# Kernel tuning notes

Hardware: AMD Instinct MI355X
Metric: run time of the kernel (lower is better)

The kernel has to match this reference:

```python
import jax, jax.numpy as jnp
import numpy as np

B, H, W, K, A = 4096, 32, 32, 20, 4


def setup_inputs() -> dict:
    key = jax.random.key(0)
    k_wall, k_agent, k_goal, k_phi, k_l1, k_l2 = jax.random.split(key, 6)
    # obs channels: 0 = wall/feature map (random), 1 = one-hot agent pos, 2 = one-hot goal pos
    walls = jax.random.uniform(k_wall, (B, H, W), dtype=jnp.float32)
    agent_idx = jax.random.randint(k_agent, (B,), 0, H * W)
    goal_idx = jax.random.randint(k_goal, (B,), 0, H * W)
    agent = jax.nn.one_hot(agent_idx, H * W, dtype=jnp.float32).reshape(B, H, W)
    goal = jax.nn.one_hot(goal_idx, H * W, dtype=jnp.float32).reshape(B, H, W)
    obs = jnp.stack([walls, agent, goal], axis=-1)  # (B,H,W,3)
    obs_flat = obs.reshape(B, H * W * 3)
    din = H * W * 3
    return {
        "obs_flat": obs_flat,
        "Phi_w": jax.random.normal(k_phi, (din, 2 * H * W), dtype=jnp.float32) * 0.02,
        "Phi_b": jnp.zeros((2 * H * W,), jnp.float32),
        "L1_w": jax.random.normal(k_l1, (36, 16), dtype=jnp.float32) * 0.1,
        "L1_b": jnp.zeros((16,), jnp.float32),
        "L2_w": jax.random.normal(k_l2, (16, A), dtype=jnp.float32) * 0.1,
        "L2_b": jnp.zeros((A,), jnp.float32),
    }


def _mvprop(r, p):
    # K-step value propagation: V <- max(V, r + p*(best 4-neighbor V - r))
    # p = sigmoid(...) >= 0, so max over the 4 shifted nv values equals nv of the max shift.
    def body(V, _):
        pv = jnp.pad(V, ((0, 0), (1, 1), (1, 1)))
        nbr = jnp.maximum(
            jnp.maximum(pv[:, :-2, 1:-1], pv[:, 2:, 1:-1]),   # up, down
            jnp.maximum(pv[:, 1:-1, :-2], pv[:, 1:-1, 2:]),   # left, right
        )
        return jnp.maximum(V, r + p * (nbr - r)), None
    V, _ = jax.lax.scan(body, r, None, length=K)
    return V


def reference(obs_flat, Phi_w, Phi_b, L1_w, L1_b, L2_w, L2_b):
    b = obs_flat.shape[0]
    obs = obs_flat.reshape(b, H, W, 3)
    phi = jax.nn.sigmoid(obs_flat @ Phi_w + Phi_b).reshape(b, H, W, 2)
    r, p = phi[..., 0], phi[..., 1]
    V = _mvprop(r, p)  # (b,H,W)
    obs_val = jnp.concatenate([obs, V[..., None]], axis=-1)  # (b,H,W,4)
    padded = jnp.pad(obs_val, ((0, 0), (1, 1), (1, 1), (0, 0)))
    # agent position: exactly one nonzero in channel 1 per sample -> argmax
    idx = jnp.argmax(obs[..., 1].reshape(b, -1), axis=1)
    pi, pj = idx // W, idx % W
    # 3x3 neighborhood around agent in padded grid (start = pos+1-1 = pos)
    def slice_one(ov, i, j):
        return jax.lax.dynamic_slice(ov, (i, j, 0), (3, 3, 4))
    sel = jax.vmap(slice_one)(padded, pi, pj)  # (b,3,3,4)
    h = jax.nn.relu(sel.reshape(b, 36) @ L1_w + L1_b)
    logit = h @ L2_w + L2_b
    return logit
```

## Files before the change

kernel.cpp:

```cpp
#include <hip/hip_runtime.h>
#include <hip/hip_fp16.h>

#define BATCH 4096
#define HH 32
#define WW 32
#define KPROP 20
#define NACT 4
#define DIN 3072
#define DPHI 2048
#define HWC 1024
#define KC 1024
#define TILE_ELEMS (16 * KC)

typedef _Float16 h8_t __attribute__((ext_vector_type(8)));
typedef _Float16 h4_t __attribute__((ext_vector_type(4)));
typedef float f32x4 __attribute__((ext_vector_type(4)));

__device__ inline float sigmoidf(float x) { return 1.0f / (1.0f + __expf(-x)); }

__device__ inline float dpp_shr1(float x) {
    return __int_as_float(__builtin_amdgcn_update_dpp(
        0, __float_as_int(x), 0x111, 0xF, 0xF, true));
}
__device__ inline float dpp_shl1(float x) {
    return __int_as_float(__builtin_amdgcn_update_dpp(
        0, __float_as_int(x), 0x101, 0xF, 0xF, true));
}

__device__ inline size_t pack_off(int row, int k) {
    return (size_t)(row >> 4) * TILE_ELEMS + (k >> 3) * 128 + (row & 15) * 8 + (k & 7);
}

__global__ __launch_bounds__(256) void prep_fused_kernel(
    const float* __restrict__ obs,
    const float* __restrict__ Phi_w,
    _Float16* __restrict__ A_pack,
    _Float16* __restrict__ B_pack,
    _Float16* __restrict__ Pag,
    int* __restrict__ aidx, int* __restrict__ gidx)
{
    if (blockIdx.x < BATCH) {
        const int t = blockIdx.x * 256 + threadIdx.x;
        const int b = t >> 8;
        const int c0 = (t & 255) * 4;
        const float* src = obs + (size_t)b * DIN + 3 * c0;
        const float4 f0 = *(const float4*)(src);
        const float4 f1 = *(const float4*)(src + 4);
        const float4 f2 = *(const float4*)(src + 8);
        h4_t w;
        w[0] = (_Float16)f0.x; w[1] = (_Float16)f0.w;
        w[2] = (_Float16)f1.z; w[3] = (_Float16)f2.y;
        *(h4_t*)(A_pack + pack_off(b, c0)) = w;
        if (f0.y > 0.5f) aidx[b] = c0;
        if (f1.x > 0.5f) aidx[b] = c0 + 1;
        if (f1.w > 0.5f) aidx[b] = c0 + 2;
        if (f2.z > 0.5f) aidx[b] = c0 + 3;
        if (f0.z > 0.5f) gidx[b] = c0;
        if (f1.y > 0.5f) gidx[b] = c0 + 1;
        if (f2.x > 0.5f) gidx[b] = c0 + 2;
        if (f2.w > 0.5f) gidx[b] = c0 + 3;
    } else {
        const int bid = blockIdx.x - BATCH;
        const int ni = bid & 63;
        const int ci = bid >> 6;
        const int tx = threadIdx.x & 31;
        const int ty = threadIdx.x >> 5;
        #pragma unroll
        for (int s = 0; s < 4; s++) {
            const int r = ty + 8 * s;
            const int c = ci * 32 + r;
            const int n = ni * 32 + tx;
            const float w0 = Phi_w[(size_t)(3 * c) * DPHI + n];
            Pag[(size_t)c * DPHI + n]         = (_Float16)Phi_w[(size_t)(3 * c + 1) * DPHI + n];
            Pag[(size_t)(HWC + c) * DPHI + n] = (_Float16)Phi_w[(size_t)(3 * c + 2) * DPHI + n];
            B_pack[pack_off(n, c)] = (_Float16)w0;
        }
    }
}

__global__ __launch_bounds__(256) void gemm_pre_kernel(
    const _Float16* __restrict__ A_pack,
    const _Float16* __restrict__ B_pack,
    const float* __restrict__ bias,
    _Float16* __restrict__ pre)
{
    const int tid  = threadIdx.x;
    const int lane = tid & 63;
    const int wid  = tid >> 6;
    const int m0 = blockIdx.y * 64;
    const int n0 = blockIdx.x * 256 + wid * 64;
    const int lm = lane & 15;
    const int kq = lane >> 4;

    const _Float16* Abase = A_pack + (size_t)(blockIdx.y * 4) * TILE_ELEMS + 8 * lane;
    const _Float16* Bbase = B_pack + (size_t)(blockIdx.x * 16 + wid * 4) * TILE_ELEMS + 8 * lane;

    f32x4 acc[4][4] = {};
    h8_t a0[4], b0[4], a1[4], b1[4];

    #pragma unroll
    for (int i = 0; i < 4; i++) {
        a0[i] = *(const h8_t*)(Abase + i * TILE_ELEMS);
        b0[i] = *(const h8_t*)(Bbase + i * TILE_ELEMS);
        a1[i] = *(const h8_t*)(Abase + i * TILE_ELEMS + 32 * 16);
        b1[i] = *(const h8_t*)(Bbase + i * TILE_ELEMS + 32 * 16);
    }

    for (int k0 = 0; k0 < KC; k0 += 64) {
        #pragma unroll
        for (int mt = 0; mt < 4; mt++)
            #pragma unroll
            for (int nt = 0; nt < 4; nt++)
                acc[mt][nt] = __builtin_amdgcn_mfma_f32_16x16x32_f16(
                    a0[mt], b0[nt], acc[mt][nt], 0, 0, 0);
        if (k0 + 64 < KC) {
            #pragma unroll
            for (int i = 0; i < 4; i++) {
                a0[i] = *(const h8_t*)(Abase + i * TILE_ELEMS + (k0 + 64) * 16);
                b0[i] = *(const h8_t*)(Bbase + i * TILE_ELEMS + (k0 + 64) * 16);
            }
        }
        #pragma unroll
        for (int mt = 0; mt < 4; mt++)
            #pragma unroll
            for (int nt = 0; nt < 4; nt++)
                acc[mt][nt] = __builtin_amdgcn_mfma_f32_16x16x32_f16(
                    a1[mt], b1[nt], acc[mt][nt], 0, 0, 0);
        if (k0 + 96 < KC) {
            #pragma unroll
            for (int i = 0; i < 4; i++) {
                a1[i] = *(const h8_t*)(Abase + i * TILE_ELEMS + (k0 + 96) * 16);
                b1[i] = *(const h8_t*)(Bbase + i * TILE_ELEMS + (k0 + 96) * 16);
            }
        }
    }

    #pragma unroll
    for (int nt = 0; nt < 4; nt++) {
        const int col = n0 + nt * 16 + lm;
        const float bcol = bias[col];
        #pragma unroll
        for (int mt = 0; mt < 4; mt++) {
            #pragma unroll
            for (int r = 0; r < 4; r++) {
                const int row = m0 + mt * 16 + kq * 4 + r;
                pre[(size_t)row * DPHI + col] = (_Float16)(acc[mt][nt][r] + bcol);
            }
        }
    }
}

__global__ __launch_bounds__(256, 4) void vprop_head_kernel(
    const _Float16* __restrict__ pre,
    const _Float16* __restrict__ Pag,
    const float* __restrict__ obs,
    const int* __restrict__ aidx,
    const int* __restrict__ gidx,
    const float* __restrict__ L1w,
    const float* __restrict__ L1b,
    const float* __restrict__ L2w,
    const float* __restrict__ L2b,
    float* __restrict__ out)
{
    __shared__ __align__(16) float Vg[4][HWC];
    __shared__ float sel[4][36], hbuf[4][16];

    const int tid  = threadIdx.x;
    const int w    = tid >> 6;
    const int lane = tid & 63;
    const int b    = blockIdx.x * 4 + w;
    const int bi   = lane & 15;
    const int bj   = lane >> 4;
    const int ai = aidx[b];
    const int gi = gidx[b];

    const _Float16* pb = pre + (size_t)b * DPHI;
    const _Float16* ra = Pag + (size_t)ai * DPHI;
    const _Float16* rg = Pag + (size_t)(HWC + gi) * DPHI;

    float v[2][8], p[2][8], a[2][8];
    #pragma unroll
    for (int r = 0; r < 2; r++) {
        const int off = 64 * (2 * bi + r) + 16 * bj;
        const h8_t ph0 = *(const h8_t*)(pb + off), ph1 = *(const h8_t*)(pb + off + 8);
        const h8_t pa0 = *(const h8_t*)(ra + off), pa1 = *(const h8_t*)(ra + off + 8);
        const h8_t pg0 = *(const h8_t*)(rg + off), pg1 = *(const h8_t*)(rg + off + 8);
        #pragma unroll
        for (int c = 0; c < 4; c++) {
            const float rv = sigmoidf((float)ph0[2*c]   + (float)pa0[2*c]   + (float)pg0[2*c]);
            const float pv = sigmoidf((float)ph0[2*c+1] + (float)pa0[2*c+1] + (float)pg0[2*c+1]);
            v[r][c] = rv; p[r][c] = pv; a[r][c] = rv * (1.0f - pv);
            const float rv2 = sigmoidf((float)ph1[2*c]   + (float)pa1[2*c]   + (float)pg1[2*c]);
            const float pv2 = sigmoidf((float)ph1[2*c+1] + (float)pa1[2*c+1] + (float)pg1[2*c+1]);
            v[r][c+4] = rv2; p[r][c+4] = pv2; a[r][c+4] = rv2 * (1.0f - pv2);
        }
    }

    for (int it = 0; it < KPROP; it++) {
        float uh[8], dh[8], lh[2], rh[2];
        #pragma unroll
        for (int c = 0; c < 8; c++) {
            uh[c] = dpp_shr1(v[1][c]);
            dh[c] = dpp_shl1(v[0][c]);
        }
        #pragma unroll
        for (int r = 0; r < 2; r++) {
            lh[r] = __shfl(v[r][7], lane - 16);
            rh[r] = __shfl(v[r][0], lane + 16);
            if (bj == 0) lh[r] = 0.0f;
            if (bj == 3) rh[r] = 0.0f;
        }
        float nb[2][8];
        #pragma unroll
        for (int c = 0; c < 8; c++) {
            const float lf0 = (c == 0) ? lh[0] : v[0][c-1];
            const float rt0 = (c == 7) ? rh[0] : v[0][c+1];
            const float lf1 = (c == 0) ? lh[1] : v[1][c-1];
            const float rt1 = (c == 7) ? rh[1] : v[1][c+1];
            nb[0][c] = fmaxf(fmaxf(uh[c], v[1][c]), fmaxf(lf0, rt0));
            nb[1][c] = fmaxf(fmaxf(v[0][c], dh[c]), fmaxf(lf1, rt1));
        }
        #pragma unroll
        for (int r = 0; r < 2; r++)
            #pragma unroll
            for (int c = 0; c < 8; c++)
                v[r][c] = fmaxf(v[r][c], fmaf(p[r][c], nb[r][c], a[r][c]));
    }

    #pragma unroll
    for (int r = 0; r < 2; r++) {
        float4 lo, hi;
        lo.x = v[r][0]; lo.y = v[r][1]; lo.z = v[r][2]; lo.w = v[r][3];
        hi.x = v[r][4]; hi.y = v[r][5]; hi.z = v[r][6]; hi.w = v[r][7];
        const int base = (2 * bi + r) * 32 + 8 * bj;
        *(float4*)&Vg[w][base]     = lo;
        *(float4*)&Vg[w][base + 4] = hi;
    }
    __syncthreads();

    const int pi = ai >> 5, pj = ai & 31;
    if (lane < 36) {
        const int cell = lane >> 2;
        const int ch = lane & 3;
        const int di = pi + cell / 3 - 1;
        const int dj = pj + cell % 3 - 1;
        float vv = 0.0f;
        if (di >= 0 && di < HH && dj >= 0 && dj < WW) {
            const int c = di * WW + dj;
            vv = (ch < 3) ? obs[(size_t)b * DIN + 3 * c + ch] : Vg[w][c];
        }
        sel[w][lane] = vv;
    }
    __syncthreads();

    if (lane < 16) {
        float h = L1b[lane];
        #pragma unroll
        for (int k = 0; k < 36; k++) h += sel[w][k] * L1w[k * 16 + lane];
        hbuf[w][lane] = fmaxf(h, 0.0f);
    }
    __syncthreads();

    if (lane < 4) {
        float o = L2b[lane];
        #pragma unroll
        for (int t = 0; t < 16; t++) o += hbuf[w][t] * L2w[t * 4 + lane];
        out[(size_t)b * NACT + lane] = o;
    }
}

extern "C" void kernel_launch(void* const* d_in, const int* in_sizes, int n_in,
                              void* d_out, int out_size, void* d_ws, size_t ws_size,
                              hipStream_t stream) {
    const float* obs   = (const float*)d_in[0];
    const float* Phi_w = (const float*)d_in[1];
    const float* Phi_b = (const float*)d_in[2];
    const float* L1w   = (const float*)d_in[3];
    const float* L1b   = (const float*)d_in[4];
    const float* L2w   = (const float*)d_in[5];
    const float* L2b   = (const float*)d_in[6];
    float* out = (float*)d_out;

    char* ws = (char*)d_ws;
    _Float16* pre    = (_Float16*)ws;
    _Float16* A_pack = (_Float16*)(ws + 16777216);
    _Float16* B_pack = (_Float16*)(ws + 25165824);
    _Float16* Pag    = (_Float16*)(ws + 29360128);
    int* aidx = (int*)(ws + 37748736);
    int* gidx = aidx + BATCH;

    prep_fused_kernel<<<BATCH + 2048, 256, 0, stream>>>(obs, Phi_w, A_pack, B_pack, Pag, aidx, gidx);
    gemm_pre_kernel<<<dim3(DPHI / 256, BATCH / 64), 256, 0, stream>>>(A_pack, B_pack, Phi_b, pre);
    vprop_head_kernel<<<BATCH / 4, 256, 0, stream>>>(pre, Pag, obs, aidx, gidx,
                                                     L1w, L1b, L2w, L2b, out);
}
```

Baseline: 167.6 us.

## Switch GEMM to 32x32x16 MFMA with 32-row packed layout and wider prep

Repacks the fp16 A and B operands into 32-row tiles and changes the GEMM from 16x16x32 MFMA to 32x32x16 MFMA, with a 2x2 grid of 32x32 accumulators per wave. This lowers instruction count and register traffic per FLOP and fits the larger MFMA shape. The prep kernel now has each thread handle 16 columns with wider 16-byte stores, and weight packing writes 4-element vector stores. Together these are meant to cut launch and store overhead. The trade-off is a different output scatter pattern and higher register pressure per thread.

```diff
diff --git a/kernel.cpp b/kernel.cpp
--- a/kernel.cpp
+++ b/kernel.cpp
@@ -10,11 +10,12 @@
 #define DPHI 2048
 #define HWC 1024
 #define KC 1024
-#define TILE_ELEMS (16 * KC)
+#define TILE32 (32 * KC)
 
 typedef _Float16 h8_t __attribute__((ext_vector_type(8)));
 typedef _Float16 h4_t __attribute__((ext_vector_type(4)));
 typedef float f32x4 __attribute__((ext_vector_type(4)));
+typedef float f32x16 __attribute__((ext_vector_type(16)));
 
 __device__ inline float sigmoidf(float x) { return 1.0f / (1.0f + __expf(-x)); }
 
@@ -27,8 +28,8 @@
         0, __float_as_int(x), 0x101, 0xF, 0xF, true));
 }
 
-__device__ inline size_t pack_off(int row, int k) {
-    return (size_t)(row >> 4) * TILE_ELEMS + (k >> 3) * 128 + (row & 15) * 8 + (k & 7);
+__device__ inline size_t pack_off32(int row, int k) {
+    return (size_t)(row >> 5) * TILE32 + (k >> 3) * 256 + (row & 31) * 8 + (k & 7);
 }
 
 __global__ __launch_bounds__(256) void prep_fused_kernel(
@@ -39,42 +40,48 @@
     _Float16* __restrict__ Pag,
     int* __restrict__ aidx, int* __restrict__ gidx)
 {
-    if (blockIdx.x < BATCH) {
-        const int t = blockIdx.x * 256 + threadIdx.x;
-        const int b = t >> 8;
-        const int c0 = (t & 255) * 4;
-        const float* src = obs + (size_t)b * DIN + 3 * c0;
-        const float4 f0 = *(const float4*)(src);
-        const float4 f1 = *(const float4*)(src + 4);
-        const float4 f2 = *(const float4*)(src + 8);
-        h4_t w;
-        w[0] = (_Float16)f0.x; w[1] = (_Float16)f0.w;
-        w[2] = (_Float16)f1.z; w[3] = (_Float16)f2.y;
-        *(h4_t*)(A_pack + pack_off(b, c0)) = w;
-        if (f0.y > 0.5f) aidx[b] = c0;
-        if (f1.x > 0.5f) aidx[b] = c0 + 1;
-        if (f1.w > 0.5f) aidx[b] = c0 + 2;
-        if (f2.z > 0.5f) aidx[b] = c0 + 3;
-        if (f0.z > 0.5f) gidx[b] = c0;
-        if (f1.y > 0.5f) gidx[b] = c0 + 1;
-        if (f2.x > 0.5f) gidx[b] = c0 + 2;
-        if (f2.w > 0.5f) gidx[b] = c0 + 3;
+    if (blockIdx.x < BATCH / 4) {
+        const int b  = blockIdx.x * 4 + (threadIdx.x >> 6);
+        const int c0 = (threadIdx.x & 63) * 16;
+        const float4* src = (const float4*)(obs + (size_t)b * DIN + 3 * c0);
+        float4 f[12];
+        #pragma unroll
+        for (int i = 0; i < 12; i++) f[i] = src[i];
+        _Float16 wv[16];
+        #pragma unroll
+        for (int g = 0; g < 4; g++) {
+            const float4 fa = f[3*g], fb = f[3*g+1], fc = f[3*g+2];
+            wv[4*g+0] = (_Float16)fa.x; wv[4*g+1] = (_Float16)fa.w;
+            wv[4*g+2] = (_Float16)fb.z; wv[4*g+3] = (_Float16)fc.y;
+            const int cc = c0 + 4 * g;
+            if (fa.y > 0.5f) aidx[b] = cc;
+            if (fb.x > 0.5f) aidx[b] = cc + 1;
+            if (fb.w > 0.5f) aidx[b] = cc + 2;
+            if (fc.z > 0.5f) aidx[b] = cc + 3;
+            if (fa.z > 0.5f) gidx[b] = cc;
+            if (fb.y > 0.5f) gidx[b] = cc + 1;
+            if (fc.x > 0.5f) gidx[b] = cc + 2;
+            if (fc.w > 0.5f) gidx[b] = cc + 3;
+        }
+        *(h8_t*)(A_pack + pack_off32(b, c0))     = *(h8_t*)&wv[0];
+        *(h8_t*)(A_pack + pack_off32(b, c0 + 8)) = *(h8_t*)&wv[8];
     } else {
-        const int bid = blockIdx.x - BATCH;
+        const int bid = blockIdx.x - BATCH / 4;
         const int ni = bid & 63;
         const int ci = bid >> 6;
         const int tx = threadIdx.x & 31;
         const int ty = threadIdx.x >> 5;
-        #pragma unroll
-        for (int s = 0; s < 4; s++) {
-            const int r = ty + 8 * s;
-            const int c = ci * 32 + r;
-            const int n = ni * 32 + tx;
-            const float w0 = Phi_w[(size_t)(3 * c) * DPHI + n];
+        const int n  = ni * 32 + tx;
+        const int c0 = ci * 32 + ty * 4;
+        h4_t wq;
+        #pragma unroll
+        for (int i = 0; i < 4; i++) {
+            const int c = c0 + i;
+            wq[i] = (_Float16)Phi_w[(size_t)(3 * c) * DPHI + n];
             Pag[(size_t)c * DPHI + n]         = (_Float16)Phi_w[(size_t)(3 * c + 1) * DPHI + n];
             Pag[(size_t)(HWC + c) * DPHI + n] = (_Float16)Phi_w[(size_t)(3 * c + 2) * DPHI + n];
-            B_pack[pack_off(n, c)] = (_Float16)w0;
-        }
+        }
+        *(h4_t*)(B_pack + pack_off32(n, c0)) = wq;
     }
 }
 
@@ -89,61 +96,71 @@
     const int wid  = tid >> 6;
     const int m0 = blockIdx.y * 64;
     const int n0 = blockIdx.x * 256 + wid * 64;
-    const int lm = lane & 15;
-    const int kq = lane >> 4;
-
-    const _Float16* Abase = A_pack + (size_t)(blockIdx.y * 4) * TILE_ELEMS + 8 * lane;
-    const _Float16* Bbase = B_pack + (size_t)(blockIdx.x * 16 + wid * 4) * TILE_ELEMS + 8 * lane;
-
-    f32x4 acc[4][4] = {};
-    h8_t a0[4], b0[4], a1[4], b1[4];
+
+    const _Float16* Abase = A_pack + (size_t)(blockIdx.y * 2) * TILE32 + 8 * lane;
+    const _Float16* Bbase = B_pack + (size_t)(blockIdx.x * 8 + wid * 2) * TILE32 + 8 * lane;
+
+    f32x16 acc[2][2] = {};
+    h8_t a0[2][2], b0[2][2], a1[2][2], b1[2][2];
 
     #pragma unroll
-    for (int i = 0; i < 4; i++) {
-        a0[i] = *(const h8_t*)(Abase + i * TILE_ELEMS);
-        b0[i] = *(const h8_t*)(Bbase + i * TILE_ELEMS);
-        a1[i] = *(const h8_t*)(Abase + i * TILE_ELEMS + 32 * 16);
-        b1[i] = *(const h8_t*)(Bbase + i * TILE_ELEMS + 32 * 16);
-    }
-
-    for (int k0 = 0; k0 < KC; k0 += 64) {
-        #pragma unroll
-        for (int mt = 0; mt < 4; mt++)
-            #pragma unroll
-            for (int nt = 0; nt < 4; nt++)
-                acc[mt][nt] = __builtin_amdgcn_mfma_f32_16x16x32_f16(
-                    a0[mt], b0[nt], acc[mt][nt], 0, 0, 0);
-        if (k0 + 64 < KC) {
-            #pragma unroll
-            for (int i = 0; i < 4; i++) {
-                a0[i] = *(const h8_t*)(Abase + i * TILE_ELEMS + (k0 + 64) * 16);
-                b0[i] = *(const h8_t*)(Bbase + i * TILE_ELEMS + (k0 + 64) * 16);
-            }
-        }
-        #pragma unroll
-        for (int mt = 0; mt < 4; mt++)
-            #pragma unroll
-            for (int nt = 0; nt < 4; nt++)
-                acc[mt][nt] = __builtin_amdgcn_mfma_f32_16x16x32_f16(
-                    a1[mt], b1[nt], acc[mt][nt], 0, 0, 0);
-        if (k0 + 96 < KC) {
-            #pragma unroll
-            for (int i = 0; i < 4; i++) {
-                a1[i] = *(const h8_t*)(Abase + i * TILE_ELEMS + (k0 + 96) * 16);
-                b1[i] = *(const h8_t*)(Bbase + i * TILE_ELEMS + (k0 + 96) * 16);
-            }
-        }
-    }
-
+    for (int t = 0; t < 2; t++)
+        #pragma unroll
+        for (int q = 0; q < 2; q++) {
+            a0[t][q] = *(const h8_t*)(Abase + t * TILE32 + q * 512);
+            b0[t][q] = *(const h8_t*)(Bbase + t * TILE32 + q * 512);
+            a1[t][q] = *(const h8_t*)(Abase + t * TILE32 + (2 + q) * 512);
+            b1[t][q] = *(const h8_t*)(Bbase + t * TILE32 + (2 + q) * 512);
+        }
+
+    for (int s0 = 0; s0 < 64; s0 += 4) {
+        #pragma unroll
+        for (int q = 0; q < 2; q++)
+            #pragma unroll
+            for (int mt = 0; mt < 2; mt++)
+                #pragma unroll
+                for (int nt = 0; nt < 2; nt++)
+                    acc[mt][nt] = __builtin_amdgcn_mfma_f32_32x32x16_f16(
+                        a0[mt][q], b0[nt][q], acc[mt][nt], 0, 0, 0);
+        if (s0 + 4 < 64) {
+            #pragma unroll
+            for (int t = 0; t < 2; t++)
+                #pragma unroll
+                for (int q = 0; q < 2; q++) {
+                    a0[t][q] = *(const h8_t*)(Abase + t * TILE32 + (s0 + 4 + q) * 512);
+                    b0[t][q] = *(const h8_t*)(Bbase + t * TILE32 + (s0 + 4 + q) * 512);
+                }
+        }
+        #pragma unroll
+        for (int q = 0; q < 2; q++)
+            #pragma unroll
+            for (int mt = 0; mt < 2; mt++)
+                #pragma unroll
+                for (int nt = 0; nt < 2; nt++)
+                    acc[mt][nt] = __builtin_amdgcn_mfma_f32_32x32x16_f16(
+                        a1[mt][q], b1[nt][q], acc[mt][nt], 0, 0, 0);
+        if (s0 + 6 < 64) {
+            #pragma unroll
+            for (int t = 0; t < 2; t++)
+                #pragma unroll
+                for (int q = 0; q < 2; q++) {
+                    a1[t][q] = *(const h8_t*)(Abase + t * TILE32 + (s0 + 6 + q) * 512);
+                    b1[t][q] = *(const h8_t*)(Bbase + t * TILE32 + (s0 + 6 + q) * 512);
+                }
+        }
+    }
+
+    const int cl  = lane & 31;
+    const int rhi = (lane >> 5) * 4;
     #pragma unroll
-    for (int nt = 0; nt < 4; nt++) {
-        const int col = n0 + nt * 16 + lm;
+    for (int nt = 0; nt < 2; nt++) {
+        const int col = n0 + nt * 32 + cl;
         const float bcol = bias[col];
         #pragma unroll
-        for (int mt = 0; mt < 4; mt++) {
-            #pragma unroll
-            for (int r = 0; r < 4; r++) {
-                const int row = m0 + mt * 16 + kq * 4 + r;
+        for (int mt = 0; mt < 2; mt++) {
+            #pragma unroll
+            for (int r = 0; r < 16; r++) {
+                const int row = m0 + mt * 32 + rhi + (r & 3) + 8 * (r >> 2);
                 pre[(size_t)row * DPHI + col] = (_Float16)(acc[mt][nt][r] + bcol);
             }
         }
@@ -289,7 +306,7 @@
     int* aidx = (int*)(ws + 37748736);
     int* gidx = aidx + BATCH;
 
-    prep_fused_kernel<<<BATCH + 2048, 256, 0, stream>>>(obs, Phi_w, A_pack, B_pack, Pag, aidx, gidx);
+    prep_fused_kernel<<<BATCH / 4 + 2048, 256, 0, stream>>>(obs, Phi_w, A_pack, B_pack, Pag, aidx, gidx);
     gemm_pre_kernel<<<dim3(DPHI / 256, BATCH / 64), 256, 0, stream>>>(A_pack, B_pack, Phi_b, pre);
     vprop_head_kernel<<<BATCH / 4, 256, 0, stream>>>(pre, Pag, obs, aidx, gidx,
                                                      L1w, L1b, L2w, L2b, out);
```

Measured after the change: 170.8 us. Within noise of the previous version (+1.9%).
